# Kernel tuning notes

Measured on AMD Instinct MI355X. Metric: run time of the kernel, lower is better.

Reference implementation:

```python
import jax, jax.numpy as jnp
import numpy as np

# SCC (sliding/overlapping channel convolution) config, matching init_kwargs
C_IN = 64
C_OUT = 64
GRP_N = 8
OVERLAP = 4
G = C_IN // GRP_N          # input_grp_unit_dim = channels per sliding window = 8
STEP = G - OVERLAP         # channel stride between consecutive output channels = 4
B, H, W = 32, 128, 128


def setup_inputs() -> dict:
    key = jax.random.key(0)
    k1, k2 = jax.random.split(key)
    x = jax.random.normal(k1, (B, C_IN, H, W), dtype=jnp.float32)
    stdv = 1.0 / np.sqrt(G)  # reset_parameters: uniform(-stdv, stdv)
    weights = jax.random.uniform(k2, (C_OUT, G), dtype=jnp.float32,
                                 minval=-stdv, maxval=stdv)
    return {"x": x, "weights": weights}


def _expand_weights(weights):
    # Scatter the (C_OUT, G) sliding-window weights into a dense (C_OUT, C_IN)
    # channel-mixing matrix. Output channel o reads input channels
    # (o*STEP + j) % C_IN for j in [0, G). This keeps the irregular channel
    # access as a tiny scatter instead of materializing a (B,O,G,H,W) gather.
    o = jnp.arange(C_OUT)[:, None]            # (C_OUT, 1)
    j = jnp.arange(G)[None, :]                # (1, G)
    idx = (o * STEP + j) % C_IN               # (C_OUT, G) wrap-around window
    w_full = jnp.zeros((C_OUT, C_IN), dtype=weights.dtype)
    w_full = w_full.at[jnp.broadcast_to(o, idx.shape), idx].add(weights)
    return w_full


def reference(x, weights):
    w_full = _expand_weights(weights)                 # (C_OUT, C_IN)
    # 1x1 spatial conv == per-pixel channel contraction
    return jnp.einsum('oc,bchw->bohw', w_full, x)     # (B, C_OUT, H, W)
```

## Files before the change

### kernel.cpp

```cpp
#include <hip/hip_runtime.h>
#include <hip/hip_bf16.h>


#define CIN   64
#define COUT  64
#define GW    8
#define STEP  4
#define HW    (128 * 128)

__global__ __launch_bounds__(256) void scc_kernel(
    const float* __restrict__ x,
    const float* __restrict__ w,
    float* __restrict__ out,
    int total_pixels)
{
    __shared__ float ws[COUT * GW];
    for (int i = threadIdx.x; i < COUT * GW; i += blockDim.x)
        ws[i] = w[i];
    __syncthreads();

    int p = blockIdx.x * blockDim.x + threadIdx.x;
    if (p >= total_pixels) return;

    int b  = p >> 14;
    int hw = p & (HW - 1);

    const float* xp = x + ((long)b * CIN) * HW + hw;
    float* op       = out + ((long)b * COUT) * HW + hw;

    float xv[CIN];
#pragma unroll
    for (int c = 0; c < CIN; ++c)
        xv[c] = xp[(long)c * HW];

#pragma unroll
    for (int o = 0; o < COUT; ++o) {
        float acc = 0.0f;
#pragma unroll
        for (int j = 0; j < GW; ++j)
            acc = fmaf(ws[o * GW + j], xv[(o * STEP + j) & (CIN - 1)], acc);
        op[(long)o * HW] = acc;
    }
}

extern "C" void kernel_launch(void* const* d_in, const int* in_sizes, int n_in,
                              void* d_out, int out_size, void* d_ws, size_t ws_size,
                              hipStream_t stream) {
    const float* x = (const float*)d_in[0];
    const float* w = (const float*)d_in[1];
    float* out     = (float*)d_out;

    const int total_pixels = 32 * HW;
    const int block = 256;
    const int grid  = (total_pixels + block - 1) / block;

    scc_kernel<<<grid, block, 0, stream>>>(x, w, out, total_pixels);
}
```

Before: 46.26 us.

## Vectorize pixels as float4 and stream channel window with rolling register buffer

Each thread now processes four consecutive pixels through float4 loads and stores, and the output loop is reordered so that output channels sharing a sliding window are computed together. Only an 8-entry float4 window of input channels stays in registers, and the next four channels are prefetched on each step, replacing the earlier approach of holding all 64 channels at once. This widens memory transactions, cuts the thread count by four, and is meant to reduce register pressure while overlapping loads with compute. It depends on the pixel count being a multiple of 1024, because the bounds check has been removed.

```diff
diff --git a/kernel.cpp b/kernel.cpp
--- a/kernel.cpp
+++ b/kernel.cpp
@@ -6,53 +6,82 @@
 #define COUT  64
 #define GW    8
 #define STEP  4
-#define HW    (128 * 128)
+#define HW4   4096
 
 __global__ __launch_bounds__(256) void scc_kernel(
-    const float* __restrict__ x,
-    const float* __restrict__ w,
-    float* __restrict__ out,
-    int total_pixels)
+    const float4* __restrict__ x,
+    const float*  __restrict__ w,
+    float4* __restrict__ out)
 {
-    __shared__ float ws[COUT * GW];
-    for (int i = threadIdx.x; i < COUT * GW; i += blockDim.x)
-        ws[i] = w[i];
+    __shared__ float4 wsv[COUT * 2];
+    {
+        float* ws = (float*)wsv;
+        for (int i = threadIdx.x; i < COUT * GW; i += blockDim.x)
+            ws[i] = w[i];
+    }
     __syncthreads();
 
-    int p = blockIdx.x * blockDim.x + threadIdx.x;
-    if (p >= total_pixels) return;
+    int t   = blockIdx.x * blockDim.x + threadIdx.x;
+    int b   = t >> 12;
+    int hw4 = t & (HW4 - 1);
 
-    int b  = p >> 14;
-    int hw = p & (HW - 1);
+    const float4* xp = x   + ((long)b * CIN) * HW4 + hw4;
+    float4*       op = out + ((long)b * COUT) * HW4 + hw4;
 
-    const float* xp = x + ((long)b * CIN) * HW + hw;
-    float* op       = out + ((long)b * COUT) * HW + hw;
-
-    float xv[CIN];
+    float4 win[8];
 #pragma unroll
-    for (int c = 0; c < CIN; ++c)
-        xv[c] = xp[(long)c * HW];
+    for (int k = 0; k < 8; ++k)
+        win[k] = xp[(long)k * HW4];
 
 #pragma unroll
-    for (int o = 0; o < COUT; ++o) {
-        float acc = 0.0f;
+    for (int wi = 0; wi < 16; ++wi) {
+        float4 nxt[4];
+        if (wi < 15) {
 #pragma unroll
-        for (int j = 0; j < GW; ++j)
-            acc = fmaf(ws[o * GW + j], xv[(o * STEP + j) & (CIN - 1)], acc);
-        op[(long)o * HW] = acc;
+            for (int k = 0; k < 4; ++k) {
+                int c = (4 * wi + 8 + k) & (CIN - 1);
+                nxt[k] = xp[(long)c * HW4];
+            }
+        }
+
+#pragma unroll
+        for (int q = 0; q < 4; ++q) {
+            int o = wi + 16 * q;
+            float4 w0 = wsv[o * 2 + 0];
+            float4 w1 = wsv[o * 2 + 1];
+            float4 a;
+            a.x = 0.f; a.y = 0.f; a.z = 0.f; a.w = 0.f;
+#pragma unroll
+            for (int j = 0; j < 8; ++j) {
+                float wt = (j < 4) ? ((const float*)&w0)[j]
+                                   : ((const float*)&w1)[j - 4];
+                float4 xv = win[(4 * wi + j) & 7];
+                a.x = fmaf(wt, xv.x, a.x);
+                a.y = fmaf(wt, xv.y, a.y);
+                a.z = fmaf(wt, xv.z, a.z);
+                a.w = fmaf(wt, xv.w, a.w);
+            }
+            op[(long)o * HW4] = a;
+        }
+
+        if (wi < 15) {
+#pragma unroll
+            for (int k = 0; k < 4; ++k)
+                win[(4 * wi + 8 + k) & 7] = nxt[k];
+        }
     }
 }
 
 extern "C" void kernel_launch(void* const* d_in, const int* in_sizes, int n_in,
                               void* d_out, int out_size, void* d_ws, size_t ws_size,
                               hipStream_t stream) {
-    const float* x = (const float*)d_in[0];
-    const float* w = (const float*)d_in[1];
-    float* out     = (float*)d_out;
+    const float4* x = (const float4*)d_in[0];
+    const float*  w = (const float*)d_in[1];
+    float4* out     = (float4*)d_out;
 
-    const int total_pixels = 32 * HW;
+    const int total_vec = 32 * HW4;
     const int block = 256;
-    const int grid  = (total_pixels + block - 1) / block;
+    const int grid  = total_vec / block;
 
-    scc_kernel<<<grid, block, 0, stream>>>(x, w, out, total_pixels);
+    scc_kernel<<<grid, block, 0, stream>>>(x, w, out);
 }
```

After: 48.71 us. +5.3%, slower.
